# Performance work log

Measured on AMD Instinct MI355X. Metric: run time of the kernel, lower is better.

The kernel has to match this reference:

```python
import jax, jax.numpy as jnp
import numpy as np

GRID_SIZE = 5
SPLINE_ORDER = 3
GRID_MIN = -1.0
GRID_MAX = 1.0
H = (GRID_MAX - GRID_MIN) / GRID_SIZE          # grid interval
G0 = GRID_MIN - SPLINE_ORDER * H               # first (extended) knot = grid[:,0]


def _basis_matrix():
    # Uniform B-spline power-basis matrix, same recurrence as the torch code.
    M = np.array([[1.0]], dtype=np.float64)
    scalar = 1.0
    for k in range(2, SPLINE_ORDER + 2):
        t1 = np.pad(M, ((0, 1), (0, 0)))
        t3 = np.pad(M, ((1, 0), (0, 0)))
        t2 = np.zeros((k - 1, k))
        t4 = np.zeros((k - 1, k))
        for i in range(k - 1):
            t2[i, i] = i + 1
            t2[i, i + 1] = k - (i + 2)
            t4[i, i] = -1.0
            t4[i, i + 1] = 1.0
        M = t1 @ t2 + t3 @ t4
        scalar *= 1.0 / (k - 1)
    return (M * scalar).astype(np.float32)

BASIS = jnp.asarray(_basis_matrix())  # (spline_order+1, spline_order+1)


def setup_inputs():
    key = jax.random.key(0)
    k1, k2, k3 = jax.random.split(key, 3)
    N, FIN, FOUT = 2048, 128, 128
    x = jax.random.normal(k1, (N, FIN), dtype=jnp.float32)
    base_weight = jax.random.normal(k2, (FOUT, FIN), dtype=jnp.float32) * 0.1
    spline_weight = jax.random.normal(k3, (FIN, FOUT, GRID_SIZE + SPLINE_ORDER), dtype=jnp.float32) * 0.1
    return {"x": x, "base_weight": base_weight, "spline_weight": spline_weight}


def _forward(x, base_weight, spline_weight):
    N, fin = x.shape
    fout = base_weight.shape[0]
    k = SPLINE_ORDER
    # base branch: SiLU activation then linear
    base_out = jax.nn.silu(x) @ base_weight.T                       # (N, fout)
    # input normalization: Hardtanh around grid center (shift=0, scale=1 for [-1,1])
    shift = (GRID_MIN + GRID_MAX) / 2.0
    scale = (GRID_MAX - GRID_MIN) / 2.0
    xn = jnp.clip((x - shift) / scale, -1.0, 1.0) * scale + shift
    # bucketize: bin index + fractional position (replaces floor/compare + torch.nonzero)
    t = (xn - G0) / H
    fl = jnp.floor(t)
    u1 = t - fl                                                     # (x - interval_floor) / interval
    idx = jnp.clip(fl.astype(jnp.int32), k, k + GRID_SIZE - 1)      # clamped knot-interval index
    cfloor = idx - k                                                # (N, fin) first control point index
    # power bases [1, u, u^2, ..., u^k] -> b-spline basis via basis matrix
    pows = u1[..., None] ** jnp.arange(k + 1, dtype=x.dtype)        # (N, fin, k+1)
    bspl = pows @ BASIS.astype(x.dtype)                             # (N, fin, k+1)
    # faithful to torch: spline_weight.view(out, in, -1) memory reinterpretation
    cp = jnp.reshape(spline_weight, (fout, fin, GRID_SIZE + k))
    gidx = cfloor[..., None] + jnp.arange(k + 1)                    # (N, fin, k+1) control point indices
    i_idx = jnp.arange(fin)[None, :, None]
    gathered = cp[:, i_idx, gidx]                                   # (fout, N, fin, k+1)
    gathered = jnp.transpose(gathered, (1, 0, 2, 3))                # (N, fout, fin, k+1)
    # faithful to torch: .view(N, in, k+1, out) memory reinterpretation
    cpr = jnp.reshape(gathered, (N, fin, k + 1, fout))
    # per-feature spline matmul then sum over in_features (KAN aggregation)
    spline_out = jnp.einsum('nij,nijo->no', bspl, cpr)              # (N, fout)
    return base_out + spline_out


def reference(x, base_weight, spline_weight):
    return _forward(x, base_weight, spline_weight)
```

## Files before the change

### kernel.cpp

```cpp
#include <hip/hip_runtime.h>
#include <hip/hip_bf16.h>
#include <math.h>

typedef __attribute__((ext_vector_type(8))) short short8;
typedef __attribute__((ext_vector_type(4))) float floatx4;

static __device__ __forceinline__ unsigned short bfbits(float f) {
    __hip_bfloat16 h = __float2bfloat16(f);
    unsigned short u;
    __builtin_memcpy(&u, &h, 2);
    return u;
}
static __device__ __forceinline__ unsigned pack2(float lo, float hi) {
    return (unsigned)bfbits(lo) | ((unsigned)bfbits(hi) << 16);
}

#define SP_STR  136
#define SBN_STR 76
#define SBB_STR 136
#define ST_STR  68
#define SC_STR  132

__global__ __launch_bounds__(256) void kan_fused(
    const float* __restrict__ x,
    const float* __restrict__ bw,
    const float* __restrict__ sw,
    float* __restrict__ out)
{
    __shared__ short sP[5 * 16 * SP_STR];
    __shared__ short sBn[2][128 * SBN_STR];
    __shared__ short sBb[32 * SBB_STR];
    __shared__ float sT[2][16 * ST_STR];
    __shared__ unsigned char sC[16 * SC_STR];

    const int tid = threadIdx.x;
    const int nb  = blockIdx.x >> 2;
    const int s   = blockIdx.x & 3;
    const int n0  = nb * 16;

    const int ar = tid >> 4;
    const int sg = tid & 15;

    const int r  = tid >> 4;
    const int i0 = (tid & 15) * 8;
    float v[8];
    *(float4*)(v)     = *(const float4*)(x + (n0 + r) * 128 + i0);
    *(float4*)(v + 4) = *(const float4*)(x + (n0 + r) * 128 + i0 + 4);

    float4 pre[8];
#pragma unroll
    for (int rr = 0; rr < 8; ++rr)
        pre[rr] = *(const float4*)(sw + (ar + 16 * rr) * 1024 + s * 64 + sg * 4);

    {
        float A5[5][8];
        unsigned char cc8[8];
#pragma unroll
        for (int i = 0; i < 8; ++i) {
            float xv = v[i];
            float si = xv / (1.0f + expf(-xv));
            float xn = fminf(fmaxf(xv, -1.0f), 1.0f);
            float t  = (xn + 2.2f) / 0.4f;
            float u  = t - floorf(t);
            int idx  = (int)floorf(t);
            idx = min(max(idx, 3), 7);
            cc8[i] = (unsigned char)(idx - 3);
            float u2 = u * u, u3 = u2 * u, om = 1.0f - u;
            A5[0][i] = om * om * om * (1.0f / 6.0f);
            A5[1][i] = 0.5f * u3 - u2 + (2.0f / 3.0f);
            A5[2][i] = -0.5f * u3 + 0.5f * u2 + 0.5f * u + (1.0f / 6.0f);
            A5[3][i] = u3 * (1.0f / 6.0f);
            A5[4][i] = si;
        }
#pragma unroll
        for (int g = 0; g < 5; ++g) {
            unsigned p0 = pack2(A5[g][0], A5[g][1]);
            unsigned p1 = pack2(A5[g][2], A5[g][3]);
            unsigned p2 = pack2(A5[g][4], A5[g][5]);
            unsigned p3 = pack2(A5[g][6], A5[g][7]);
            *(uint4*)(&sP[(g * 16 + r) * SP_STR + i0]) = make_uint4(p0, p1, p2, p3);
        }
        *(unsigned*)(&sC[r * SC_STR + i0])     = cc8[0] | (cc8[1]<<8) | (cc8[2]<<16) | (cc8[3]<<24);
        *(unsigned*)(&sC[r * SC_STR + i0 + 4]) = cc8[4] | (cc8[5]<<8) | (cc8[6]<<16) | (cc8[7]<<24);
    }

    const int w = tid >> 6, l = tid & 63;
    const int m = l & 15, q = l >> 4;
    const int gn  = tid >> 4;
    const int go2 = tid & 15;

    uint2 pk[8];
#pragma unroll
    for (int rr = 0; rr < 8; ++rr)
        pk[rr] = make_uint2(pack2(pre[rr].x, pre[rr].y), pack2(pre[rr].z, pre[rr].w));

    float racc0 = 0.f, racc1 = 0.f;
    float4 bpre[4];

#pragma unroll
    for (int t = 0; t < 4; ++t) {
        const int p = t & 1;
#pragma unroll
        for (int rr = 0; rr < 8; ++rr)
            *(uint2*)(&sBn[p][(ar + 16 * rr) * SBN_STR + sg * 4]) = pk[rr];
        __syncthreads();

        if (t < 3) {
#pragma unroll
            for (int rr = 0; rr < 8; ++rr)
                pre[rr] = *(const float4*)(sw + (ar + 16 * rr) * 1024 + (s + 4 * (t + 1)) * 64 + sg * 4);
        } else {
#pragma unroll
            for (int i = 0; i < 4; ++i) {
                int e = i * 256 + tid;
                bpre[i] = *(const float4*)(bw + (32 * s + (e >> 5)) * 128 + (e & 31) * 4);
            }
        }

        if (t > 0) {
            int oh  = 8 * s + (go2 >> 1);
            int c   = sC[gn * SC_STR + 32 * (t - 1) + oh];
            int rel = 8 * (go2 >> 1) + c + 2 * (go2 & 1);
            racc0 += sT[1 - p][gn * ST_STR + rel];
            racc1 += sT[1 - p][gn * ST_STR + rel + 1];
        }

        floatx4 acc = {0.f, 0.f, 0.f, 0.f};
#pragma unroll
        for (int kk = 0; kk < 4; ++kk) {
            short8 af = *(const short8*)(&sP[(t * 16 + m) * SP_STR + q * 8 + kk * 32]);
            short8 bf;
#pragma unroll
            for (int j2 = 0; j2 < 8; ++j2)
                bf[j2] = sBn[p][(kk * 32 + q * 8 + j2) * SBN_STR + 16 * w + m];
            acc = __builtin_amdgcn_mfma_f32_16x16x32_bf16(af, bf, acc, 0, 0, 0);
        }
#pragma unroll
        for (int rr = 0; rr < 4; ++rr)
            sT[p][(q * 4 + rr) * ST_STR + 16 * w + m] = acc[rr];

        if (t < 3) {
#pragma unroll
            for (int rr = 0; rr < 8; ++rr)
                pk[rr] = make_uint2(pack2(pre[rr].x, pre[rr].y), pack2(pre[rr].z, pre[rr].w));
        }
    }

#pragma unroll
    for (int i = 0; i < 4; ++i) {
        int e = i * 256 + tid;
        *(uint2*)(&sBb[(e >> 5) * SBB_STR + (e & 31) * 4]) =
            make_uint2(pack2(bpre[i].x, bpre[i].y), pack2(bpre[i].z, bpre[i].w));
    }
    __syncthreads();

    {
        int oh  = 8 * s + (go2 >> 1);
        int c   = sC[gn * SC_STR + 32 * 3 + oh];
        int rel = 8 * (go2 >> 1) + c + 2 * (go2 & 1);
        racc0 += sT[1][gn * ST_STR + rel];
        racc1 += sT[1][gn * ST_STR + rel + 1];
    }

    if (w < 2) {
        floatx4 acc = {0.f, 0.f, 0.f, 0.f};
#pragma unroll
        for (int kk = 0; kk < 4; ++kk) {
            short8 af = *(const short8*)(&sP[(4 * 16 + m) * SP_STR + q * 8 + kk * 32]);
            short8 bf = *(const short8*)(&sBb[(16 * w + m) * SBB_STR + q * 8 + kk * 32]);
            acc = __builtin_amdgcn_mfma_f32_16x16x32_bf16(af, bf, acc, 0, 0, 0);
        }
#pragma unroll
        for (int rr = 0; rr < 4; ++rr)
            sT[0][(q * 4 + rr) * ST_STR + 16 * w + m] = acc[rr];
    }
    __syncthreads();

    racc0 += sT[0][gn * ST_STR + 2 * go2];
    racc1 += sT[0][gn * ST_STR + 2 * go2 + 1];

    *(float2*)(out + (n0 + gn) * 128 + 32 * s + 2 * go2) = make_float2(racc0, racc1);
}

extern "C" void kernel_launch(void* const* d_in, const int* in_sizes, int n_in,
                              void* d_out, int out_size, void* d_ws, size_t ws_size,
                              hipStream_t stream) {
    const float* x  = (const float*)d_in[0];
    const float* bw = (const float*)d_in[1];
    const float* sw = (const float*)d_in[2];
    float* out = (float*)d_out;
    kan_fused<<<dim3(512), dim3(256), 0, stream>>>(x, bw, sw, out);
}
```

Measured before the change: 63.42 us.

## Give each wave its own spline-weight chunk and drop the per-step barriers

Each of the four waves now handles one of the four column chunks independently. Each wave keeps a private 64-row LDS tile, loads the two 64-row halves of its spline weights into registers, and runs four accumulators over 16 columns each. This replaces the old four-step loop that needed a __syncthreads per step. The base-weight MFMA operands now go straight from global memory into registers on waves 2-3, skipping the LDS staging. The kernel also adds a minimum-two-blocks occupancy hint. The cost is more live registers (32 float4 prefetches plus 8 for base weights), which may cause spills or lower occupancy. The second-half LDS write reuses the same tile with no barrier, relying on in-wave ordering.

Measured after the change: 63.19 us. Within noise of the previous version (-0.4%).

```diff
diff --git a/kernel.cpp b/kernel.cpp
--- a/kernel.cpp
+++ b/kernel.cpp
@@ -4,6 +4,11 @@
 
 typedef __attribute__((ext_vector_type(8))) short short8;
 typedef __attribute__((ext_vector_type(4))) float floatx4;
+
+typedef unsigned int uint_a   __attribute__((may_alias));
+typedef uint2        uint2_a  __attribute__((may_alias));
+typedef uint4        uint4_a  __attribute__((may_alias));
+typedef short8       short8_a __attribute__((may_alias));
 
 static __device__ __forceinline__ unsigned short bfbits(float f) {
     __hip_bfloat16 h = __float2bfloat16(f);
@@ -16,21 +21,21 @@
 }
 
 #define SP_STR  136
-#define SBN_STR 76
-#define SBB_STR 136
+#define SBN_STR 68
 #define ST_STR  68
+#define STB_STR 36
 #define SC_STR  132
 
-__global__ __launch_bounds__(256) void kan_fused(
+__global__ __launch_bounds__(256, 2) void kan_fused(
     const float* __restrict__ x,
     const float* __restrict__ bw,
     const float* __restrict__ sw,
     float* __restrict__ out)
 {
     __shared__ short sP[5 * 16 * SP_STR];
-    __shared__ short sBn[2][128 * SBN_STR];
-    __shared__ short sBb[32 * SBB_STR];
-    __shared__ float sT[2][16 * ST_STR];
+    __shared__ short sBn[4 * 64 * SBN_STR];
+    __shared__ float sT[4 * 16 * ST_STR];
+    __shared__ float sTb[16 * STB_STR];
     __shared__ unsigned char sC[16 * SC_STR];
 
     const int tid = threadIdx.x;
@@ -38,8 +43,8 @@
     const int s   = blockIdx.x & 3;
     const int n0  = nb * 16;
 
-    const int ar = tid >> 4;
-    const int sg = tid & 15;
+    const int w = tid >> 6, l = tid & 63;
+    const int m = l & 15, q = l >> 4;
 
     const int r  = tid >> 4;
     const int i0 = (tid & 15) * 8;
@@ -47,10 +52,22 @@
     *(float4*)(v)     = *(const float4*)(x + (n0 + r) * 128 + i0);
     *(float4*)(v + 4) = *(const float4*)(x + (n0 + r) * 128 + i0 + 4);
 
-    float4 pre[8];
-#pragma unroll
-    for (int rr = 0; rr < 8; ++rr)
-        pre[rr] = *(const float4*)(sw + (ar + 16 * rr) * 1024 + s * 64 + sg * 4);
+    const int cc = s + 4 * w;
+    const float* swp = sw + cc * 64 + m * 4;
+    float4 pre[16];
+#pragma unroll
+    for (int rr = 0; rr < 16; ++rr)
+        pre[rr] = *(const float4*)(swp + (q + 4 * rr) * 1024);
+
+    float4 bw8[8];
+    if (w >= 2) {
+        const float* bwp = bw + (32 * s + 16 * (w - 2) + m) * 128 + q * 8;
+#pragma unroll
+        for (int kk = 0; kk < 4; ++kk) {
+            bw8[2 * kk]     = *(const float4*)(bwp + kk * 32);
+            bw8[2 * kk + 1] = *(const float4*)(bwp + kk * 32 + 4);
+        }
+    }
 
     {
         float A5[5][8];
@@ -78,107 +95,98 @@
             unsigned p1 = pack2(A5[g][2], A5[g][3]);
             unsigned p2 = pack2(A5[g][4], A5[g][5]);
             unsigned p3 = pack2(A5[g][6], A5[g][7]);
-            *(uint4*)(&sP[(g * 16 + r) * SP_STR + i0]) = make_uint4(p0, p1, p2, p3);
-        }
-        *(unsigned*)(&sC[r * SC_STR + i0])     = cc8[0] | (cc8[1]<<8) | (cc8[2]<<16) | (cc8[3]<<24);
-        *(unsigned*)(&sC[r * SC_STR + i0 + 4]) = cc8[4] | (cc8[5]<<8) | (cc8[6]<<16) | (cc8[7]<<24);
-    }
-
-    const int w = tid >> 6, l = tid & 63;
-    const int m = l & 15, q = l >> 4;
-    const int gn  = tid >> 4;
-    const int go2 = tid & 15;
-
-    uint2 pk[8];
-#pragma unroll
-    for (int rr = 0; rr < 8; ++rr)
-        pk[rr] = make_uint2(pack2(pre[rr].x, pre[rr].y), pack2(pre[rr].z, pre[rr].w));
-
-    float racc0 = 0.f, racc1 = 0.f;
-    float4 bpre[4];
-
-#pragma unroll
-    for (int t = 0; t < 4; ++t) {
-        const int p = t & 1;
-#pragma unroll
-        for (int rr = 0; rr < 8; ++rr)
-            *(uint2*)(&sBn[p][(ar + 16 * rr) * SBN_STR + sg * 4]) = pk[rr];
-        __syncthreads();
-
-        if (t < 3) {
-#pragma unroll
-            for (int rr = 0; rr < 8; ++rr)
-                pre[rr] = *(const float4*)(sw + (ar + 16 * rr) * 1024 + (s + 4 * (t + 1)) * 64 + sg * 4);
-        } else {
-#pragma unroll
-            for (int i = 0; i < 4; ++i) {
-                int e = i * 256 + tid;
-                bpre[i] = *(const float4*)(bw + (32 * s + (e >> 5)) * 128 + (e & 31) * 4);
-            }
-        }
-
-        if (t > 0) {
-            int oh  = 8 * s + (go2 >> 1);
-            int c   = sC[gn * SC_STR + 32 * (t - 1) + oh];
-            int rel = 8 * (go2 >> 1) + c + 2 * (go2 & 1);
-            racc0 += sT[1 - p][gn * ST_STR + rel];
-            racc1 += sT[1 - p][gn * ST_STR + rel + 1];
-        }
-
-        floatx4 acc = {0.f, 0.f, 0.f, 0.f};
+            *(uint4_a*)(&sP[(g * 16 + r) * SP_STR + i0]) = make_uint4(p0, p1, p2, p3);
+        }
+        *(uint_a*)(&sC[r * SC_STR + i0])     = cc8[0] | (cc8[1]<<8) | (cc8[2]<<16) | (cc8[3]<<24);
+        *(uint_a*)(&sC[r * SC_STR + i0 + 4]) = cc8[4] | (cc8[5]<<8) | (cc8[6]<<16) | (cc8[7]<<24);
+    }
+
+#pragma unroll
+    for (int rr = 0; rr < 16; ++rr)
+        *(uint2_a*)(&sBn[(w * 64 + q + 4 * rr) * SBN_STR + m * 4]) =
+            make_uint2(pack2(pre[rr].x, pre[rr].y), pack2(pre[rr].z, pre[rr].w));
+
+    __syncthreads();
+
+    float4 pre2[16];
+#pragma unroll
+    for (int rr = 0; rr < 16; ++rr)
+        pre2[rr] = *(const float4*)(swp + (64 + q + 4 * rr) * 1024);
+
+    const short* tile = &sBn[w * 64 * SBN_STR];
+    const short* ap   = &sP[(w * 16 + m) * SP_STR + q * 8];
+    floatx4 acc[4] = {{0.f,0.f,0.f,0.f},{0.f,0.f,0.f,0.f},
+                      {0.f,0.f,0.f,0.f},{0.f,0.f,0.f,0.f}};
+
+#pragma unroll
+    for (int kh = 0; kh < 2; ++kh) {
+        short8 af = *(const short8_a*)(ap + kh * 32);
+#pragma unroll
+        for (int cg = 0; cg < 4; ++cg) {
+            short8 bf;
+#pragma unroll
+            for (int j2 = 0; j2 < 8; ++j2)
+                bf[j2] = tile[(kh * 32 + q * 8 + j2) * SBN_STR + cg * 16 + m];
+            acc[cg] = __builtin_amdgcn_mfma_f32_16x16x32_bf16(af, bf, acc[cg], 0, 0, 0);
+        }
+    }
+
+#pragma unroll
+    for (int rr = 0; rr < 16; ++rr)
+        *(uint2_a*)(&sBn[(w * 64 + q + 4 * rr) * SBN_STR + m * 4]) =
+            make_uint2(pack2(pre2[rr].x, pre2[rr].y), pack2(pre2[rr].z, pre2[rr].w));
+
+#pragma unroll
+    for (int kh = 0; kh < 2; ++kh) {
+        short8 af = *(const short8_a*)(ap + (2 + kh) * 32);
+#pragma unroll
+        for (int cg = 0; cg < 4; ++cg) {
+            short8 bf;
+#pragma unroll
+            for (int j2 = 0; j2 < 8; ++j2)
+                bf[j2] = tile[(kh * 32 + q * 8 + j2) * SBN_STR + cg * 16 + m];
+            acc[cg] = __builtin_amdgcn_mfma_f32_16x16x32_bf16(af, bf, acc[cg], 0, 0, 0);
+        }
+    }
+
+#pragma unroll
+    for (int cg = 0; cg < 4; ++cg)
+#pragma unroll
+        for (int rr = 0; rr < 4; ++rr)
+            sT[(w * 16 + q * 4 + rr) * ST_STR + cg * 16 + m] = acc[cg][rr];
+
+    if (w >= 2) {
+        const short* ap4 = &sP[(4 * 16 + m) * SP_STR + q * 8];
+        floatx4 ab = {0.f, 0.f, 0.f, 0.f};
 #pragma unroll
         for (int kk = 0; kk < 4; ++kk) {
-            short8 af = *(const short8*)(&sP[(t * 16 + m) * SP_STR + q * 8 + kk * 32]);
+            short8 af = *(const short8_a*)(ap4 + kk * 32);
+            uint4 pb = make_uint4(pack2(bw8[2*kk].x,   bw8[2*kk].y),
+                                  pack2(bw8[2*kk].z,   bw8[2*kk].w),
+                                  pack2(bw8[2*kk+1].x, bw8[2*kk+1].y),
+                                  pack2(bw8[2*kk+1].z, bw8[2*kk+1].w));
             short8 bf;
-#pragma unroll
-            for (int j2 = 0; j2 < 8; ++j2)
-                bf[j2] = sBn[p][(kk * 32 + q * 8 + j2) * SBN_STR + 16 * w + m];
-            acc = __builtin_amdgcn_mfma_f32_16x16x32_bf16(af, bf, acc, 0, 0, 0);
+            __builtin_memcpy(&bf, &pb, 16);
+            ab = __builtin_amdgcn_mfma_f32_16x16x32_bf16(af, bf, ab, 0, 0, 0);
         }
 #pragma unroll
         for (int rr = 0; rr < 4; ++rr)
-            sT[p][(q * 4 + rr) * ST_STR + 16 * w + m] = acc[rr];
-
-        if (t < 3) {
-#pragma unroll
-            for (int rr = 0; rr < 8; ++rr)
-                pk[rr] = make_uint2(pack2(pre[rr].x, pre[rr].y), pack2(pre[rr].z, pre[rr].w));
-        }
-    }
-
-#pragma unroll
-    for (int i = 0; i < 4; ++i) {
-        int e = i * 256 + tid;
-        *(uint2*)(&sBb[(e >> 5) * SBB_STR + (e & 31) * 4]) =
-            make_uint2(pack2(bpre[i].x, bpre[i].y), pack2(bpre[i].z, bpre[i].w));
-    }
+            sTb[(q * 4 + rr) * STB_STR + 16 * (w - 2) + m] = ab[rr];
+    }
+
     __syncthreads();
 
-    {
-        int oh  = 8 * s + (go2 >> 1);
-        int c   = sC[gn * SC_STR + 32 * 3 + oh];
+    const int gn = tid >> 4, go2 = tid & 15;
+    const int oh = 8 * s + (go2 >> 1);
+    float racc0 = sTb[gn * STB_STR + 2 * go2];
+    float racc1 = sTb[gn * STB_STR + 2 * go2 + 1];
+#pragma unroll
+    for (int j = 0; j < 4; ++j) {
+        int c   = sC[gn * SC_STR + 32 * j + oh];
         int rel = 8 * (go2 >> 1) + c + 2 * (go2 & 1);
-        racc0 += sT[1][gn * ST_STR + rel];
-        racc1 += sT[1][gn * ST_STR + rel + 1];
-    }
-
-    if (w < 2) {
-        floatx4 acc = {0.f, 0.f, 0.f, 0.f};
-#pragma unroll
-        for (int kk = 0; kk < 4; ++kk) {
-            short8 af = *(const short8*)(&sP[(4 * 16 + m) * SP_STR + q * 8 + kk * 32]);
-            short8 bf = *(const short8*)(&sBb[(16 * w + m) * SBB_STR + q * 8 + kk * 32]);
-            acc = __builtin_amdgcn_mfma_f32_16x16x32_bf16(af, bf, acc, 0, 0, 0);
-        }
-#pragma unroll
-        for (int rr = 0; rr < 4; ++rr)
-            sT[0][(q * 4 + rr) * ST_STR + 16 * w + m] = acc[rr];
-    }
-    __syncthreads();
-
-    racc0 += sT[0][gn * ST_STR + 2 * go2];
-    racc1 += sT[0][gn * ST_STR + 2 * go2 + 1];
-
+        racc0 += sT[(j * 16 + gn) * ST_STR + rel];
+        racc1 += sT[(j * 16 + gn) * ST_STR + rel + 1];
+    }
     *(float2*)(out + (n0 + gn) * 128 + 32 * s + 2 * go2) = make_float2(racc0, racc1);
 }
 
```
